# Kernel optimization log

Hardware: AMD Instinct MI355X
Metric: run time of the kernel (lower is better)

The kernel has to match this reference:

```python
import jax, jax.numpy as jnp
import numpy as np

B, L = 32, 200
NUM_C, NUM_D, DIM_V = 256, 32, 128


def setup_inputs() -> dict:
    key = jax.random.key(0)
    ks = jax.random.split(key, 20)
    def n(k, shape, s=0.05):
        return (jax.random.normal(k, shape) * s).astype(jnp.float32)
    return {
        "c_seq": jax.random.randint(ks[0], (B, L), 0, NUM_C),
        "d_seq": jax.random.randint(ks[1], (B, L), 0, NUM_D),
        "r_seq": jax.random.uniform(ks[2], (B, L), dtype=jnp.float32),
        # learned params
        "X": n(ks[3], (NUM_C * NUM_D, DIM_V), 0.1),      # Embedding table
        "v_r": n(ks[4], (DIM_V,), 0.1),
        "v_beta": n(ks[5], (DIM_V,), 0.1),
        # GRU (torch layout: gates [r|z|n] stacked)
        "W_ih": n(ks[6], (3 * DIM_V, 2 * DIM_V)),
        "W_hh": n(ks[7], (3 * DIM_V, DIM_V)),
        "b_ih": n(ks[8], (3 * DIM_V,)),
        "b_hh": n(ks[9], (3 * DIM_V,)),
        # linear_1: dim_v -> dim_v -> num_d (dropout = identity in eval)
        "W1a": n(ks[10], (DIM_V, DIM_V)), "b1a": n(ks[11], (DIM_V,)),
        "W1b": n(ks[12], (NUM_D, DIM_V)), "b1b": n(ks[13], (NUM_D,)),
        # linear_2: 3*dim_v -> dim_v -> num_d
        "W2a": n(ks[14], (DIM_V, 3 * DIM_V)), "b2a": n(ks[15], (DIM_V,)),
        "W2b": n(ks[16], (NUM_D, DIM_V)), "b2b": n(ks[17], (NUM_D,)),
    }


def reference(c_seq, d_seq, r_seq, X, v_r, v_beta, W_ih, W_hh, b_ih, b_hh,
              W1a, b1a, W1b, b1b, W2a, b2a, W2b, b2b):
    # embedding lookup: x = c + num_c * d
    v_x_seq = X[c_seq + NUM_C * d_seq]              # [B,L,V]
    v_r_seq = r_seq[..., None] * v_r                # [B,L,V]
    gru_in = jnp.concatenate([v_x_seq, v_r_seq], -1)  # [B,L,2V]

    # GRU (torch semantics), precompute input projections
    gx = jnp.einsum('blf,gf->blg', gru_in, W_ih) + b_ih  # [B,L,3V]

    def gru_step(h, gx_t):
        gh = h @ W_hh.T + b_hh
        xr, xz, xn = jnp.split(gx_t, 3, axis=-1)
        hr, hz, hn = jnp.split(gh, 3, axis=-1)
        r = jax.nn.sigmoid(xr + hr)
        z = jax.nn.sigmoid(xz + hz)
        n_ = jnp.tanh(xn + r * hn)
        h = (1.0 - z) * n_ + z * h
        return h, h

    h0 = jnp.zeros((B, DIM_V), dtype=gru_in.dtype)
    _, h_seq = jax.lax.scan(gru_step, h0, jnp.swapaxes(gx, 0, 1))
    h_seq = jnp.swapaxes(h_seq, 0, 1)               # [B,L,V]

    # linear_1 (dropout is identity at inference)
    alpha_seq = jax.nn.relu(h_seq @ W1a.T + b1a) @ W1b.T + b1b  # [B,L,num_d]

    # sequential memory update; one-hot gather/scatter expressed as true
    # gather C[b, c_t, d_t] and row scatter C[b, c_t, :] = new_c (same math)
    bidx = jnp.arange(B)

    def mem_step(C, inp):
        c_t, d_t, vx_t, vr_t = inp
        beta = C[bidx, c_t, d_t]                    # [B]
        v_beta_t = beta[:, None] * v_beta           # [B,V]
        zcat = jnp.concatenate([v_beta_t, vx_t, vr_t], -1)  # [B,3V]
        new_c = jax.nn.relu(zcat @ W2a.T + b2a) @ W2b.T + b2b  # [B,num_d]
        C = C.at[bidx, c_t].set(new_c)
        return C, C

    C0 = jnp.zeros((B, NUM_C, NUM_D), jnp.float32)
    _, C_seq = jax.lax.scan(
        mem_step, C0,
        (jnp.swapaxes(c_seq, 0, 1), jnp.swapaxes(d_seq, 0, 1),
         jnp.swapaxes(v_x_seq, 0, 1), jnp.swapaxes(v_r_seq, 0, 1)))
    C_seq = jnp.swapaxes(C_seq, 0, 1)               # [B,L,num_c,num_d]
    return alpha_seq, h_seq, C_seq
```

## Files before the change

### kernel.cpp

```cpp
#include <hip/hip_runtime.h>
#include <hip/hip_bf16.h>

typedef unsigned short u16;
typedef unsigned int u32;
typedef short short8 __attribute__((ext_vector_type(8)));
typedef float f32x4 __attribute__((ext_vector_type(4)));

constexpr int BATCH = 32, L = 200, NUM_C = 256, NUM_D = 32, V = 128;
constexpr int G3 = 384;
constexpr int KQ = 512;
constexpr int ROWS = BATCH * L;
constexpr size_t ALPHA_OFF = 0;
constexpr size_t H_OFF = (size_t)ROWS * NUM_D;
constexpr size_t C_OFF = H_OFF + (size_t)ROWS * V;

__device__ inline u16 f2bf(float f) {
  __hip_bfloat16 h = __float2bfloat16(f);
  return __builtin_bit_cast(u16, h);
}
__device__ inline float bf2f(u16 u) { u32 x = ((u32)u) << 16; return __builtin_bit_cast(float, x); }

__device__ inline void cvt32(const float* __restrict__ src, u16* __restrict__ dst) {
#pragma unroll
  for (int j0 = 0; j0 < 32; j0 += 4) {
    const f32x4 v = *(const f32x4*)(src + j0);
    ushort4 s;
    s.x = f2bf(v[0]); s.y = f2bf(v[1]); s.z = f2bf(v[2]); s.w = f2bf(v[3]);
    *(ushort4*)(dst + j0) = s;
  }
}
__device__ inline short8 ldfrag(const float* __restrict__ p) {
  const f32x4 a = *(const f32x4*)p, b = *(const f32x4*)(p + 4);
  short8 s;
  s[0] = (short)f2bf(a[0]); s[1] = (short)f2bf(a[1]);
  s[2] = (short)f2bf(a[2]); s[3] = (short)f2bf(a[3]);
  s[4] = (short)f2bf(b[0]); s[5] = (short)f2bf(b[1]);
  s[6] = (short)f2bf(b[2]); s[7] = (short)f2bf(b[3]);
  return s;
}

__global__ __launch_bounds__(256) void k1(
    const int* __restrict__ c_seq, const int* __restrict__ d_seq,
    const float* __restrict__ r_seq, const float* __restrict__ X,
    const float* __restrict__ v_r, const float* __restrict__ W_ih,
    const float* __restrict__ W2a, const float* __restrict__ b_ih,
    const float* __restrict__ b2a, float* __restrict__ Qout)
{
  __shared__ __align__(16) u16 Als[64][144];
  __shared__ __align__(16) u16 Bls[64][144];
  const int tid = threadIdx.x;
  const int mt = blockIdx.x, nt = blockIdx.y;
  const int lane = tid & 63, w = tid >> 6;
  const int q = lane >> 4, m = lane & 15;

  f32x4 acc[4];
#pragma unroll
  for (int i = 0; i < 4; ++i) acc[i] = (f32x4)0.0f;

  const int r0 = tid >> 2;
  const int kc = (tid & 3) * 32;
  const int rowg = mt * 64 + r0;
  const int gcolB = nt * 64 + r0;

  for (int s = 0; s < 2; ++s) {
    if (s) __syncthreads();
    if (s == 0) {
      const int idx = c_seq[rowg] + NUM_C * d_seq[rowg];
      cvt32(X + (size_t)idx * V + kc, &Als[r0][kc]);
    } else {
      const float rv = r_seq[rowg];
#pragma unroll
      for (int j0 = 0; j0 < 32; j0 += 4) {
        const f32x4 v = *(const f32x4*)(v_r + kc + j0);
        ushort4 sv;
        sv.x = f2bf(rv * v[0]); sv.y = f2bf(rv * v[1]);
        sv.z = f2bf(rv * v[2]); sv.w = f2bf(rv * v[3]);
        *(ushort4*)&Als[r0][kc + j0] = sv;
      }
    }
    {
      const float* src = (gcolB < G3)
        ? (W_ih + (size_t)gcolB * 256 + s * 128 + kc)
        : (W2a + (size_t)(gcolB - G3) * G3 + V + s * 128 + kc);
      cvt32(src, &Bls[r0][kc]);
    }
    __syncthreads();
#pragma unroll
    for (int c = 0; c < 4; ++c) {
      const short8 af = *(const short8*)&Als[w * 16 + m][32 * c + 8 * q];
#pragma unroll
      for (int i = 0; i < 4; ++i) {
        const short8 bf = *(const short8*)&Bls[i * 16 + m][32 * c + 8 * q];
        acc[i] = __builtin_amdgcn_mfma_f32_16x16x32_bf16(af, bf, acc[i], 0, 0, 0);
      }
    }
  }
#pragma unroll
  for (int i = 0; i < 4; ++i) {
    const int col = nt * 64 + i * 16 + m;
    const float bias = (col < G3) ? b_ih[col] : b2a[col - G3];
#pragma unroll
    for (int r = 0; r < 4; ++r) {
      const int rowo = mt * 64 + w * 16 + q * 4 + r;
      Qout[(size_t)rowo * KQ + col] = acc[i][r] + bias;
    }
  }
}

union ShK2 {
  struct { u16 h_bf[2][V]; } g;
  struct { float C[NUM_C * NUM_D]; int cb[L]; int db[L]; float u[V]; } s;
};

__global__ __launch_bounds__(256, 1) void k2(
    const int* __restrict__ c_seq, const int* __restrict__ d_seq,
    const float* __restrict__ W_hh, const float* __restrict__ b_hh,
    const float* __restrict__ W2a, const float* __restrict__ v_beta,
    const float* __restrict__ W2b, const float* __restrict__ b2b,
    const float* __restrict__ Q, float* __restrict__ out)
{
  __shared__ __align__(16) ShK2 sh;
  const int tid = threadIdx.x;
  const int l = tid & 63, w = tid >> 6, q = l >> 4, m = l & 15;

  if (blockIdx.x < 32) {
    const int b = blockIdx.x;
    if (tid < V) sh.g.h_bf[0][tid] = 0;
    __syncthreads();
    short8 wf[6][4];
    float bhh[6]; int gcol[6];
#pragma unroll
    for (int i = 0; i < 6; ++i) {
      const int g = (w + 4 * i) * 16 + m;
      gcol[i] = g;
      bhh[i] = b_hh[g];
#pragma unroll
      for (int c = 0; c < 4; ++c)
        wf[i][c] = ldfrag(W_hh + (size_t)g * V + 32 * c + 8 * q);
    }
    const float* Qb = Q + (size_t)b * L * KQ;
    float* outh = out + H_OFF + (size_t)b * L * V;
    const int vi0 = 16 * w + m, vi1 = 64 + 16 * w + m;
    float hold[2] = {0.f, 0.f};
    float hst[2] = {0.f, 0.f};
    const f32x4 z4 = (f32x4)0.0f;
    float gxA[6], gxB[6];
#pragma unroll
    for (int i = 0; i < 6; ++i) gxA[i] = Qb[gcol[i]];
#pragma unroll
    for (int i = 0; i < 6; ++i) gxB[i] = Qb[KQ + gcol[i]];

    auto step = [&](int t, float (&gx)[6]) {
      const int rs = t & 1, wsl = rs ^ 1;
      short8 af[4];
#pragma unroll
      for (int c = 0; c < 4; ++c)
        af[c] = *(const short8*)&sh.g.h_bf[rs][32 * c + 8 * q];
      if (t > 0 && q == 0) {
        outh[(size_t)(t - 1) * V + vi0] = hst[0];
        outh[(size_t)(t - 1) * V + vi1] = hst[1];
      }
      f32x4 acc[6];
#pragma unroll
      for (int i = 0; i < 6; ++i)
        acc[i] = __builtin_amdgcn_mfma_f32_16x16x32_bf16(af[0], wf[i][0], z4, 0, 0, 0);
#pragma unroll
      for (int c = 1; c < 4; ++c)
#pragma unroll
        for (int i = 0; i < 6; ++i)
          acc[i] = __builtin_amdgcn_mfma_f32_16x16x32_bf16(af[c], wf[i][c], acc[i], 0, 0, 0);
      float hnew[2];
#pragma unroll
      for (int s = 0; s < 2; ++s) {
        const float xr = gx[0 + s] + acc[0 + s][0] + bhh[0 + s];
        const float xz = gx[2 + s] + acc[2 + s][0] + bhh[2 + s];
        const float ghn = acc[4 + s][0] + bhh[4 + s];
        const float r = 1.f / (1.f + __expf(-xr));
        const float z = 1.f / (1.f + __expf(-xz));
        const float xn = gx[4 + s] + r * ghn;
        const float e = __expf(2.f * xn);
        const float n = 1.f - 2.f / (e + 1.f);
        hnew[s] = (1.f - z) * n + z * hold[s];
      }
      if (q == 0) {
        sh.g.h_bf[wsl][vi0] = f2bf(hnew[0]);
        sh.g.h_bf[wsl][vi1] = f2bf(hnew[1]);
      }
      hold[0] = hnew[0]; hold[1] = hnew[1];
      hst[0] = hnew[0]; hst[1] = hnew[1];
      if (t + 2 < L) {
        const float* Qr = Qb + (size_t)(t + 2) * KQ;
#pragma unroll
        for (int i = 0; i < 6; ++i) gx[i] = Qr[gcol[i]];
      }
      __builtin_amdgcn_s_waitcnt(0xc07f);
      __builtin_amdgcn_s_barrier();
    };

    for (int t = 0; t < L; t += 2) {
      step(t, gxA);
      step(t + 1, gxB);
    }
    if (q == 0) {
      outh[(size_t)(L - 1) * V + vi0] = hst[0];
      outh[(size_t)(L - 1) * V + vi1] = hst[1];
    }
  } else {
    const int b = blockIdx.x - 32;
    for (int i = tid; i < NUM_C * NUM_D; i += 256) sh.s.C[i] = 0.f;
    if (tid < L) { sh.s.cb[tid] = c_seq[b * L + tid]; sh.s.db[tid] = d_seq[b * L + tid]; }
    if (tid < V) {
      float a = 0.f;
      const float* wr = W2a + (size_t)tid * G3;
      for (int k = 0; k < V; ++k) a += wr[k] * v_beta[k];
      sh.s.u[tid] = a;
    }
    __syncthreads();
    if (tid >= 64) return;
    float ureg[4][8];
#pragma unroll
    for (int c = 0; c < 4; ++c)
#pragma unroll
      for (int j = 0; j < 8; ++j) ureg[c][j] = sh.s.u[32 * c + 8 * q + j];
    short8 wbf[2][4];
    float bb[2];
#pragma unroll
    for (int tt = 0; tt < 2; ++tt) {
#pragma unroll
      for (int c = 0; c < 4; ++c)
        wbf[tt][c] = ldfrag(W2b + (size_t)(tt * 16 + m) * V + 32 * c + 8 * q);
      bb[tt] = b2b[tt * 16 + m];
    }
    const float* Pb = Q + (size_t)b * L * KQ + G3;
    float* outc = out + C_OFF + (size_t)b * L * (NUM_C * NUM_D);
    f32x4 pcur[4][2];
#pragma unroll
    for (int c = 0; c < 4; ++c) {
      pcur[c][0] = *(const f32x4*)(Pb + 32 * c + 8 * q);
      pcur[c][1] = *(const f32x4*)(Pb + 32 * c + 8 * q + 4);
    }
    float beta = 0.f;
    int ct = sh.s.cb[0];
    for (int t = 0; t < L; ++t) {
      __builtin_amdgcn_s_waitcnt(0xc07f);
      const int tn = (t + 1 < L) ? t + 1 : t;
      const int cn = sh.s.cb[tn], dn = sh.s.db[tn];
      const float bpre = sh.s.C[cn * NUM_D + dn];
      short8 af[4];
#pragma unroll
      for (int c = 0; c < 4; ++c) {
        short8 a;
#pragma unroll
        for (int j = 0; j < 8; ++j) {
          const float p = (j < 4) ? pcur[c][0][j] : pcur[c][1][j - 4];
          const float hv = fmaxf(beta * ureg[c][j] + p, 0.f);
          a[j] = (short)f2bf(hv);
        }
        af[c] = a;
      }
      const float* Pn = Pb + (size_t)tn * KQ;
#pragma unroll
      for (int c = 0; c < 4; ++c) {
        pcur[c][0] = *(const f32x4*)(Pn + 32 * c + 8 * q);
        pcur[c][1] = *(const f32x4*)(Pn + 32 * c + 8 * q + 4);
      }
      f32x4 a0 = (f32x4)0.0f, a1 = (f32x4)0.0f;
#pragma unroll
      for (int c = 0; c < 4; ++c) {
        a0 = __builtin_amdgcn_mfma_f32_16x16x32_bf16(af[c], wbf[0][c], a0, 0, 0, 0);
        a1 = __builtin_amdgcn_mfma_f32_16x16x32_bf16(af[c], wbf[1][c], a1, 0, 0, 0);
      }
      const float n0 = a0[0] + bb[0], n1 = a1[0] + bb[1];
      if (q == 0) {
        sh.s.C[ct * NUM_D + m] = n0;
        sh.s.C[ct * NUM_D + 16 + m] = n1;
        float* oc = outc + (size_t)t * (NUM_C * NUM_D) + ct * NUM_D;
        oc[m] = n0;
        oc[16 + m] = n1;
      }
      float nb = bpre;
      if (cn == ct) nb = (dn < 16) ? __shfl(n0, dn, 64) : __shfl(n1, dn - 16, 64);
      beta = nb;
      ct = cn;
    }
  }
}

union ShK3 {
  struct { int cb[L]; float stage[L][NUM_D]; } f;
  struct { u16 hls[64][144]; u16 hid[64][144]; } a;
};

__global__ __launch_bounds__(256) void k3(
    const int* __restrict__ c_seq, const float* __restrict__ W1a,
    const float* __restrict__ b1a, const float* __restrict__ W1b,
    const float* __restrict__ b1b, float* __restrict__ out)
{
  __shared__ __align__(16) ShK3 sh;
  const int tid = threadIdx.x;
  if (blockIdx.x < 256) {
    const int blk = blockIdx.x;
    const int b = blk >> 3, cbase = (blk & 7) * 32;
    if (tid < L) sh.f.cb[tid] = c_seq[b * L + tid];
    __syncthreads();
    if (tid < L) {
      const int c = sh.f.cb[tid];
      if (c >= cbase && c < cbase + 32) {
        const float* src = out + C_OFF + ((size_t)b * L + tid) * (NUM_C * NUM_D) + (size_t)c * NUM_D;
#pragma unroll
        for (int j = 0; j < 8; ++j)
          *(f32x4*)&sh.f.stage[tid][j * 4] = *(const f32x4*)(src + j * 4);
      }
    }
    __syncthreads();
    const int cl = tid >> 3, dq = (tid & 7) * 4;
    const int myc = cbase + cl;
    float* base = out + C_OFF + (size_t)b * L * (NUM_C * NUM_D) + (size_t)myc * NUM_D + dq;
    f32x4 cur = (f32x4)0.0f;
    for (int t = 0; t < L; ++t) {
      if (sh.f.cb[t] == myc) cur = *(const f32x4*)&sh.f.stage[t][dq];
      *(f32x4*)base = cur;
      base += NUM_C * NUM_D;
    }
  } else {
    const int ab = blockIdx.x - 256;
    const int l = tid & 63, w = tid >> 6, q = l >> 4, m = l & 15;
    {
      const int r0 = tid >> 2, kc = (tid & 3) * 32;
      cvt32(out + H_OFF + (size_t)(ab * 64 + r0) * V + kc, &sh.a.hls[r0][kc]);
    }
    __syncthreads();
    f32x4 acc1[8];
#pragma unroll
    for (int i = 0; i < 8; ++i) acc1[i] = (f32x4)0.0f;
#pragma unroll
    for (int c = 0; c < 4; ++c) {
      const short8 af = *(const short8*)&sh.a.hls[w * 16 + m][32 * c + 8 * q];
#pragma unroll
      for (int i = 0; i < 8; ++i) {
        const short8 bf = ldfrag(W1a + (size_t)(i * 16 + m) * V + 32 * c + 8 * q);
        acc1[i] = __builtin_amdgcn_mfma_f32_16x16x32_bf16(af, bf, acc1[i], 0, 0, 0);
      }
    }
#pragma unroll
    for (int i = 0; i < 8; ++i) {
      const int col = i * 16 + m;
      const float bias = b1a[col];
#pragma unroll
      for (int r = 0; r < 4; ++r)
        sh.a.hid[w * 16 + q * 4 + r][col] = f2bf(fmaxf(acc1[i][r] + bias, 0.f));
    }
    __syncthreads();
    f32x4 acc2[2];
    acc2[0] = (f32x4)0.0f; acc2[1] = (f32x4)0.0f;
#pragma unroll
    for (int c = 0; c < 4; ++c) {
      const short8 af = *(const short8*)&sh.a.hid[w * 16 + m][32 * c + 8 * q];
#pragma unroll
      for (int tt = 0; tt < 2; ++tt) {
        const short8 bf = ldfrag(W1b + (size_t)(tt * 16 + m) * V + 32 * c + 8 * q);
        acc2[tt] = __builtin_amdgcn_mfma_f32_16x16x32_bf16(af, bf, acc2[tt], 0, 0, 0);
      }
    }
#pragma unroll
    for (int tt = 0; tt < 2; ++tt) {
      const int col = tt * 16 + m;
      const float bias = b1b[col];
#pragma unroll
      for (int r = 0; r < 4; ++r) {
        const int row = ab * 64 + w * 16 + q * 4 + r;
        out[ALPHA_OFF + (size_t)row * NUM_D + col] = acc2[tt][r] + bias;
      }
    }
  }
}

extern "C" void kernel_launch(void* const* d_in, const int* in_sizes, int n_in,
                              void* d_out, int out_size, void* d_ws, size_t ws_size,
                              hipStream_t stream) {
  const int*   c_seq  = (const int*)d_in[0];
  const int*   d_seq  = (const int*)d_in[1];
  const float* r_seq  = (const float*)d_in[2];
  const float* X      = (const float*)d_in[3];
  const float* v_r    = (const float*)d_in[4];
  const float* v_beta = (const float*)d_in[5];
  const float* W_ih   = (const float*)d_in[6];
  const float* W_hh   = (const float*)d_in[7];
  const float* b_ih   = (const float*)d_in[8];
  const float* b_hh   = (const float*)d_in[9];
  const float* W1a    = (const float*)d_in[10];
  const float* b1a    = (const float*)d_in[11];
  const float* W1b    = (const float*)d_in[12];
  const float* b1b    = (const float*)d_in[13];
  const float* W2a    = (const float*)d_in[14];
  const float* b2a    = (const float*)d_in[15];
  const float* W2b    = (const float*)d_in[16];
  const float* b2b    = (const float*)d_in[17];
  float* out = (float*)d_out;
  float* Q = (float*)d_ws;

  k1<<<dim3(100, 8), 256, 0, stream>>>(c_seq, d_seq, r_seq, X, v_r, W_ih, W2a, b_ih, b2a, Q);
  k2<<<64, 256, 0, stream>>>(c_seq, d_seq, W_hh, b_hh, W2a, v_beta, W2b, b2b, Q, out);
  k3<<<356, 256, 0, stream>>>(c_seq, W1a, b1a, W1b, b1b, out);
}
```

Measured before the change: 394.5 us.

## Parallelize memory recurrence via same-concept dependency chains and iterative rounds

The serial 200-step memory-update loop is replaced by a dependency analysis: each step's beta depends only on the most recent earlier step with the same concept. Predecessor links and the maximum chain depth are computed in shared memory. All steps are then re-evaluated in parallel across four waves for depth+1 rounds until the values settle. Each step's new row is written out at the end. This removes the long serial latency chain of the memory blocks, in exchange for redundant recomputation each round and extra barriers. The benefit depends on chain depth staying small.

```diff
diff --git a/kernel.cpp b/kernel.cpp
--- a/kernel.cpp
+++ b/kernel.cpp
@@ -10,6 +10,7 @@
 constexpr int G3 = 384;
 constexpr int KQ = 512;
 constexpr int ROWS = BATCH * L;
+constexpr int TP = 208;
 constexpr size_t ALPHA_OFF = 0;
 constexpr size_t H_OFF = (size_t)ROWS * NUM_D;
 constexpr size_t C_OFF = H_OFF + (size_t)ROWS * V;
@@ -109,7 +110,12 @@
 
 union ShK2 {
   struct { u16 h_bf[2][V]; } g;
-  struct { float C[NUM_C * NUM_D]; int cb[L]; int db[L]; float u[V]; } s;
+  struct {
+    int cb[TP]; int db[TP]; int sp[TP];
+    float nr[TP][36];
+    float u[V];
+    int maxd;
+  } s;
 };
 
 __global__ __launch_bounds__(256, 1) void k2(
@@ -207,16 +213,42 @@
     }
   } else {
     const int b = blockIdx.x - 32;
-    for (int i = tid; i < NUM_C * NUM_D; i += 256) sh.s.C[i] = 0.f;
-    if (tid < L) { sh.s.cb[tid] = c_seq[b * L + tid]; sh.s.db[tid] = d_seq[b * L + tid]; }
+    for (int i = tid; i < TP; i += 256) {
+      int c = -1, d = 0;
+      if (i < L) { c = c_seq[b * L + i]; d = d_seq[b * L + i]; }
+      sh.s.cb[i] = c; sh.s.db[i] = d; sh.s.sp[i] = -1;
+    }
     if (tid < V) {
       float a = 0.f;
       const float* wr = W2a + (size_t)tid * G3;
       for (int k = 0; k < V; ++k) a += wr[k] * v_beta[k];
       sh.s.u[tid] = a;
     }
-    __syncthreads();
-    if (tid >= 64) return;
+    if (tid == 0) sh.s.maxd = 0;
+    __syncthreads();
+    {
+      const int c = tid;
+      int prev = -1;
+      for (int t4 = 0; t4 < L; t4 += 4) {
+        const int4 v = *(const int4*)&sh.s.cb[t4];
+        if (v.x == c) { sh.s.sp[t4 + 0] = prev; prev = t4 + 0; }
+        if (v.y == c) { sh.s.sp[t4 + 1] = prev; prev = t4 + 1; }
+        if (v.z == c) { sh.s.sp[t4 + 2] = prev; prev = t4 + 2; }
+        if (v.w == c) { sh.s.sp[t4 + 3] = prev; prev = t4 + 3; }
+      }
+    }
+    __syncthreads();
+    {
+      int dmx = 0;
+      for (int t = tid; t < L; t += 256) {
+        int dd = 0, s = sh.s.sp[t];
+        while (s >= 0) { ++dd; s = sh.s.sp[s]; }
+        dmx = dmx > dd ? dmx : dd;
+      }
+      atomicMax(&sh.s.maxd, dmx);
+    }
+    __syncthreads();
+    const int rounds = sh.s.maxd + 1;
     float ureg[4][8];
 #pragma unroll
     for (int c = 0; c < 4; ++c)
@@ -231,57 +263,50 @@
         wbf[tt][c] = ldfrag(W2b + (size_t)(tt * 16 + m) * V + 32 * c + 8 * q);
       bb[tt] = b2b[tt * 16 + m];
     }
-    const float* Pb = Q + (size_t)b * L * KQ + G3;
+    const f32x4 z4 = (f32x4)0.0f;
+    for (int rd = 0; rd < rounds; ++rd) {
+      for (int ti = w; ti < 13; ti += 4) {
+        const int t0 = ti * 16;
+        const int tt = t0 + m;
+        const bool ok = tt < L;
+        const int spv = ok ? sh.s.sp[tt] : -1;
+        const int dbv = ok ? sh.s.db[tt] : 0;
+        const float beta = (spv >= 0) ? sh.s.nr[spv][dbv] : 0.f;
+        const float* pr = Q + ((size_t)b * L + tt) * KQ + G3 + 8 * q;
+        short8 af[4];
+#pragma unroll
+        for (int c = 0; c < 4; ++c) {
+          const f32x4 p0 = ok ? *(const f32x4*)(pr + 32 * c) : (f32x4)0.0f;
+          const f32x4 p1 = ok ? *(const f32x4*)(pr + 32 * c + 4) : (f32x4)0.0f;
+          short8 a;
+#pragma unroll
+          for (int j = 0; j < 8; ++j) {
+            const float pv = (j < 4) ? p0[j] : p1[j - 4];
+            a[j] = (short)f2bf(fmaxf(beta * ureg[c][j] + pv, 0.f));
+          }
+          af[c] = a;
+        }
+        f32x4 a0 = z4, a1 = z4;
+#pragma unroll
+        for (int c = 0; c < 4; ++c) {
+          a0 = __builtin_amdgcn_mfma_f32_16x16x32_bf16(af[c], wbf[0][c], a0, 0, 0, 0);
+          a1 = __builtin_amdgcn_mfma_f32_16x16x32_bf16(af[c], wbf[1][c], a1, 0, 0, 0);
+        }
+#pragma unroll
+        for (int r = 0; r < 4; ++r) {
+          const int tr = t0 + q * 4 + r;
+          sh.s.nr[tr][m]      = a0[r] + bb[0];
+          sh.s.nr[tr][16 + m] = a1[r] + bb[1];
+        }
+      }
+      __syncthreads();
+    }
     float* outc = out + C_OFF + (size_t)b * L * (NUM_C * NUM_D);
-    f32x4 pcur[4][2];
-#pragma unroll
-    for (int c = 0; c < 4; ++c) {
-      pcur[c][0] = *(const f32x4*)(Pb + 32 * c + 8 * q);
-      pcur[c][1] = *(const f32x4*)(Pb + 32 * c + 8 * q + 4);
-    }
-    float beta = 0.f;
-    int ct = sh.s.cb[0];
-    for (int t = 0; t < L; ++t) {
-      __builtin_amdgcn_s_waitcnt(0xc07f);
-      const int tn = (t + 1 < L) ? t + 1 : t;
-      const int cn = sh.s.cb[tn], dn = sh.s.db[tn];
-      const float bpre = sh.s.C[cn * NUM_D + dn];
-      short8 af[4];
-#pragma unroll
-      for (int c = 0; c < 4; ++c) {
-        short8 a;
-#pragma unroll
-        for (int j = 0; j < 8; ++j) {
-          const float p = (j < 4) ? pcur[c][0][j] : pcur[c][1][j - 4];
-          const float hv = fmaxf(beta * ureg[c][j] + p, 0.f);
-          a[j] = (short)f2bf(hv);
-        }
-        af[c] = a;
-      }
-      const float* Pn = Pb + (size_t)tn * KQ;
-#pragma unroll
-      for (int c = 0; c < 4; ++c) {
-        pcur[c][0] = *(const f32x4*)(Pn + 32 * c + 8 * q);
-        pcur[c][1] = *(const f32x4*)(Pn + 32 * c + 8 * q + 4);
-      }
-      f32x4 a0 = (f32x4)0.0f, a1 = (f32x4)0.0f;
-#pragma unroll
-      for (int c = 0; c < 4; ++c) {
-        a0 = __builtin_amdgcn_mfma_f32_16x16x32_bf16(af[c], wbf[0][c], a0, 0, 0, 0);
-        a1 = __builtin_amdgcn_mfma_f32_16x16x32_bf16(af[c], wbf[1][c], a1, 0, 0, 0);
-      }
-      const float n0 = a0[0] + bb[0], n1 = a1[0] + bb[1];
-      if (q == 0) {
-        sh.s.C[ct * NUM_D + m] = n0;
-        sh.s.C[ct * NUM_D + 16 + m] = n1;
-        float* oc = outc + (size_t)t * (NUM_C * NUM_D) + ct * NUM_D;
-        oc[m] = n0;
-        oc[16 + m] = n1;
-      }
-      float nb = bpre;
-      if (cn == ct) nb = (dn < 16) ? __shfl(n0, dn, 64) : __shfl(n1, dn - 16, 64);
-      beta = nb;
-      ct = cn;
+    const int j4 = (tid & 7) * 4;
+    for (int t = tid >> 3; t < L; t += 32) {
+      const int c = sh.s.cb[t];
+      float* oc = outc + (size_t)t * (NUM_C * NUM_D) + c * NUM_D + j4;
+      *(f32x4*)oc = *(const f32x4*)&sh.s.nr[t][j4];
     }
   }
 }
```

Measured after the change: 395.1 us. Within noise of the previous version (+0.2%).
